# Optimization experiments

Hardware: AMD Instinct MI355X
Metric: run time of the kernel (lower is better)

Reference implementation:

```python
import jax, jax.numpy as jnp
import numpy as np

POOLED_SIZES = [11, 8, 6, 4]
Q_POOLED = 2
NUM_HEADS = 2
EPS_ROUND = 1e-3  # module's self.eps used only in aspect-ratio rounding
LN_EPS = 1e-5     # torch nn.LayerNorm default


def _pool_mat(in_size, out_size):
    # PyTorch adaptive_avg_pool1d windows: start=floor(i*in/out), end=ceil((i+1)*in/out)
    M = np.zeros((out_size, in_size), np.float32)
    for i in range(out_size):
        s = (i * in_size) // out_size
        e = -(((-(i + 1)) * in_size) // out_size)
        M[i, s:e] = 1.0 / (e - s)
    return jnp.asarray(M)


def _bilinear_mat(in_size, out_size):
    # PyTorch F.interpolate bilinear, align_corners=False (half-pixel centers, clamped)
    scale = in_size / out_size
    M = np.zeros((out_size, in_size), np.float32)
    for i in range(out_size):
        src = (i + 0.5) * scale - 0.5
        src = min(max(src, 0.0), in_size - 1)
        i0 = int(np.floor(src))
        i1 = min(i0 + 1, in_size - 1)
        w = src - i0
        M[i, i0] += 1.0 - w
        M[i, i1] += w
    return jnp.asarray(M)


def _ln(x, g, b):
    m = jnp.mean(x, axis=-1, keepdims=True)
    v = jnp.mean((x - m) ** 2, axis=-1, keepdims=True)
    return (x - m) * jax.lax.rsqrt(v + LN_EPS) * g + b


def _out_size(p, H, W):
    if W >= H:
        return (p, round(W * p / H + EPS_ROUND))
    return (round(H * p / W + EPS_ROUND), p)


def setup_inputs() -> dict:
    key = jax.random.key(0)
    ks = jax.random.split(key, 12)
    B, C, H, W = 8, 32, 512, 512
    L = len(POOLED_SIZES)
    return {
        "x": jax.random.normal(ks[0], (B, C, H, W), jnp.float32),
        "q_w": jax.random.normal(ks[1], (C, C), jnp.float32) * 0.05,
        "q_b": jax.random.normal(ks[2], (C,), jnp.float32) * 0.01,
        "kv_w": jax.random.normal(ks[3], (C, 2 * C), jnp.float32) * 0.05,
        "kv_b": jax.random.normal(ks[4], (2 * C,), jnp.float32) * 0.01,
        "proj_w": jax.random.normal(ks[5], (C, C), jnp.float32) * 0.05,
        "proj_b": jax.random.normal(ks[6], (C,), jnp.float32) * 0.01,
        "norm_g": jnp.ones((C,), jnp.float32),
        "norm_b": jnp.zeros((C,), jnp.float32),
        "dconv_w": jax.random.normal(ks[7], (L, C, 1, 3, 3), jnp.float32) * 0.05,  # OIHW depthwise, stacked per level
        "dconv_b": jax.random.normal(ks[8], (L, C), jnp.float32) * 0.01,
        "H": 512,
        "W": 512,
    }


def reference(x, q_w, q_b, kv_w, kv_b, proj_w, proj_b, norm_g, norm_b, dconv_w, dconv_b, H, W):
    B, C = x.shape[0], x.shape[1]
    nh = NUM_HEADS
    hd = C // nh
    scale = hd ** (-0.5)

    # ---- query branch: adaptive pool to ~2x2, then linear ----
    qh, qw = _out_size(Q_POOLED, H, W)
    qp = jnp.einsum('ph,bchw,qw->bcpq', _pool_mat(H, qh), x, _pool_mat(W, qw))  # (B,C,qh,qw)
    qt = qp.reshape(B, C, -1).transpose(0, 2, 1)                               # (B,Nq,C)
    q = (qt @ q_w + q_b).reshape(B, -1, nh, hd).transpose(0, 2, 1, 3)          # (B,nh,Nq,hd)

    # ---- KV pyramid: adaptive pool + depthwise conv residual per level ----
    toks = []
    for i, p in enumerate(POOLED_SIZES):
        ph, pw = _out_size(p, H, W)
        pooled = jnp.einsum('ph,bchw,qw->bcpq', _pool_mat(H, ph), x, _pool_mat(W, pw))
        conv = jax.lax.conv_general_dilated(
            pooled, dconv_w[i], window_strides=(1, 1), padding='SAME',
            feature_group_count=C, dimension_numbers=('NCHW', 'OIHW', 'NCHW'))
        conv = conv + dconv_b[i][None, :, None, None]
        toks.append((pooled + conv).reshape(B, C, -1))
    toks = jnp.concatenate(toks, axis=2).transpose(0, 2, 1)  # (B,Nk,C), Nk=237
    toks = _ln(toks, norm_g, norm_b)

    kv = (toks @ kv_w + kv_b).reshape(B, -1, 2, nh, hd).transpose(2, 0, 3, 1, 4)
    k, v = kv[0], kv[1]                                       # (B,nh,Nk,hd)

    # ---- small-scale attention ----
    attn = jax.nn.softmax(jnp.einsum('bhqd,bhkd->bhqk', q, k) * scale, axis=-1)
    o = jnp.einsum('bhqk,bhkd->bhqd', attn, v).transpose(0, 2, 1, 3).reshape(B, -1, C)
    o = o @ proj_w + proj_b                                    # (B,Nq,C)

    # ---- bilinear upsample back to (H,W) ----
    o = o.transpose(0, 2, 1).reshape(B, C, qh, qw)
    out = jnp.einsum('hp,bcpq,wq->bchw', _bilinear_mat(qh, H), o, _bilinear_mat(qw, W))
    return out  # (B,C,H,W), same as module's to_4d output
```

## Files before the change

kernel.cpp:

```cpp
#include <hip/hip_runtime.h>
#include <math.h>

#define BB 8
#define CC 32
#define NTOK 241
#define NKV 237
#define YW 516
#define NSLOT 16

struct WS { int idx, s, e, left, slot; float ax, ay, az, aw; };

template <int P>
__device__ __forceinline__ void ws_init(WS& w, int i0, int n, int sb) {
  w.idx = i0;
  w.s = (i0 * 512) / P;
  w.e = ((i0 + 1) * 512 + P - 1) / P;
  w.left = n;
  w.slot = sb;
  w.ax = w.ay = w.az = w.aw = 0.f;
}

template <int P>
__device__ __forceinline__ void ws_step(WS& w, float4 v, int r,
                                        float* __restrict__ Y, int c4) {
  if (w.left > 0) {
    if (r >= w.s && r < w.e) {
      w.ax += v.x; w.ay += v.y; w.az += v.z; w.aw += v.w;
    }
    if (r < w.e && r + 4 >= w.e) {
      float* dst = Y + w.slot * YW + c4;
      atomicAdd(dst + 0, w.ax);
      atomicAdd(dst + 1, w.ay);
      atomicAdd(dst + 2, w.az);
      atomicAdd(dst + 3, w.aw);
      w.slot++; w.left--; w.idx++;
      int sn = (w.idx * 512) / P;
      w.e = ((w.idx + 1) * 512 + P - 1) / P;
      bool ov = (sn <= r);
      w.ax = ov ? v.x : 0.f; w.ay = ov ? v.y : 0.f;
      w.az = ov ? v.z : 0.f; w.aw = ov ? v.w : 0.f;
      w.s = sn;
    }
  }
}

__global__ __launch_bounds__(512) void pool_kernel(const float* __restrict__ x,
                                                   float* __restrict__ pooled) {
  __shared__ float Ybuf[NSLOT * YW];

  const int plane = blockIdx.x >> 1;
  const int q = blockIdx.x & 1;
  const int tid = threadIdx.x;

  for (int i = tid; i < NSLOT * YW; i += 512) Ybuf[i] = 0.f;

  const int lo = q ? 256 : 0;
  const int NIT = q ? 64 : 72;
  int i0_2, n_2, i0_11, n_11, i0_8, n_8, i0_6, n_6, i0_4, n_4;
  if (q == 0) {
    i0_2 = 0; n_2 = 1; i0_11 = 0; n_11 = 6; i0_8 = 0; n_8 = 4;
    i0_6 = 0; n_6 = 3; i0_4 = 0; n_4 = 2;
  } else {
    i0_2 = 1; n_2 = 1; i0_11 = 6; n_11 = 5; i0_8 = 4; n_8 = 4;
    i0_6 = 3; n_6 = 3; i0_4 = 2; n_4 = 2;
  }

  WS W2, W11, W8, W6, W4;
  ws_init<2>(W2, i0_2, n_2, 0);
  ws_init<11>(W11, i0_11, n_11, 1);
  ws_init<8>(W8, i0_8, n_8, 7);
  ws_init<6>(W6, i0_6, n_6, 11);
  ws_init<4>(W4, i0_4, n_4, 14);

  const int r0 = tid >> 7;
  const int c4 = (tid & 127) * 4;
  const float* xp = x + (size_t)plane * (512 * 512);

  __syncthreads();

#define LOADIT(IT) \
  (*(const float4*)(xp + (size_t)min(lo + r0 + 4 * (IT), 511) * 512 + c4))
#define PROCIT(V, IT)                                                          \
  {                                                                            \
    int r = lo + r0 + 4 * (IT);                                                \
    ws_step<2>(W2, V, r, Ybuf, c4);                                            \
    ws_step<11>(W11, V, r, Ybuf, c4);                                          \
    ws_step<8>(W8, V, r, Ybuf, c4);                                            \
    ws_step<6>(W6, V, r, Ybuf, c4);                                            \
    ws_step<4>(W4, V, r, Ybuf, c4);                                            \
  }

  float4 Av = LOADIT(0), Bv = LOADIT(1), Cv = LOADIT(2), Dv = LOADIT(3);
  for (int it = 0; it < NIT; it += 4) {
    PROCIT(Av, it);     Av = LOADIT(it + 4);
    PROCIT(Bv, it + 1); Bv = LOADIT(it + 5);
    PROCIT(Cv, it + 2); Cv = LOADIT(it + 6);
    PROCIT(Dv, it + 3); Dv = LOADIT(it + 7);
  }
#undef LOADIT
#undef PROCIT
  __syncthreads();

  const int Ps[5]  = {2, 11, 8, 6, 4};
  const int KBs[5] = {0, 4, 125, 189, 225};
  const int SBs[5] = {0, 1, 7, 11, 14};
  const int i0s[5] = {i0_2, i0_11, i0_8, i0_6, i0_4};
  const int ns[5]  = {n_2, n_11, n_8, n_6, n_4};
  int cum[6]; cum[0] = 0;
#pragma unroll
  for (int l = 0; l < 5; ++l) cum[l + 1] = cum[l] + ns[l] * Ps[l];

  if (tid < cum[5]) {
    int l = 0;
    while (tid >= cum[l + 1]) ++l;
    int P = Ps[l];
    int rel = tid - cum[l];
    int li = rel / P, j = rel - li * P;
    int i = i0s[l] + li;
    int s = (i * 512) / P, e = ((i + 1) * 512 + P - 1) / P;
    int sw = (j * 512) / P, ew = ((j + 1) * 512 + P - 1) / P;
    const float* row = &Ybuf[(SBs[l] + li) * YW];
    float t0 = 0.f, t1 = 0.f, t2 = 0.f, t3 = 0.f;
    int cc = sw;
    for (; cc + 4 <= ew; cc += 4) {
      t0 += row[cc]; t1 += row[cc + 1]; t2 += row[cc + 2]; t3 += row[cc + 3];
    }
    for (; cc < ew; ++cc) t0 += row[cc];
    float val = ((t0 + t1) + (t2 + t3)) / (float)((e - s) * (ew - sw));
    pooled[(size_t)plane * NTOK + KBs[l] + i * P + j] = val;
  }
}

__global__ __launch_bounds__(512) void attn_kernel(
    const float* __restrict__ pooled,
    const float* __restrict__ q_w, const float* __restrict__ q_b,
    const float* __restrict__ kv_w, const float* __restrict__ kv_b,
    const float* __restrict__ proj_w, const float* __restrict__ proj_b,
    const float* __restrict__ norm_g, const float* __restrict__ norm_b,
    const float* __restrict__ dconv_w, const float* __restrict__ dconv_b,
    float* __restrict__ o_out) {
  __shared__ float pl[CC * NTOK];
  __shared__ float toks[NKV][33];
  __shared__ float kvls[NKV][65];
  __shared__ float kvw[CC * 64];
  __shared__ float dw[4 * CC * 9];
  __shared__ float dbias[4 * CC];
  __shared__ float qbias[CC], kvb[64], gln[CC], bln[CC];
  __shared__ float qtok[4][CC];
  __shared__ float attno[4][33];

  const int b = blockIdx.x, tid = threadIdx.x;
  const float* plg = pooled + (size_t)b * CC * NTOK;
  for (int i = tid; i < CC * NTOK; i += 512) pl[i] = plg[i];
  for (int i = tid; i < CC * 64; i += 512) kvw[i] = kv_w[i];
  for (int i = tid; i < 4 * CC * 9; i += 512) dw[i] = dconv_w[i];
  if (tid < 4 * CC) dbias[tid] = dconv_b[tid];
  if (tid < CC) { qbias[tid] = q_b[tid]; gln[tid] = norm_g[tid]; bln[tid] = norm_b[tid]; }
  if (tid >= 64 && tid < 128) kvb[tid - 64] = kv_b[tid - 64];
  __syncthreads();

  for (int item = tid; item < NKV * CC; item += 512) {
    int t = item >> 5, c = item & 31;
    int l, p, kb_, tb;
    if (t < 121)      { l = 0; p = 11; kb_ = 4;   tb = 0; }
    else if (t < 185) { l = 1; p = 8;  kb_ = 125; tb = 121; }
    else if (t < 221) { l = 2; p = 6;  kb_ = 189; tb = 185; }
    else              { l = 3; p = 4;  kb_ = 225; tb = 221; }
    int ti = t - tb;
    int i = ti / p, j = ti - i * p;
    const float* plc = pl + c * NTOK + kb_;
    const float* w9 = dw + (l * CC + c) * 9;
    float acc = dbias[l * CC + c];
#pragma unroll
    for (int dy = -1; dy <= 1; ++dy)
#pragma unroll
      for (int dx = -1; dx <= 1; ++dx) {
        int ii = i + dy, jj = j + dx;
        if (ii >= 0 && ii < p && jj >= 0 && jj < p)
          acc += w9[(dy + 1) * 3 + (dx + 1)] * plc[ii * p + jj];
      }
    toks[t][c] = plc[i * p + j] + acc;
  }
  __syncthreads();

  if (tid < NKV) {
    float xv[32]; float m = 0.f;
#pragma unroll
    for (int c = 0; c < 32; ++c) { xv[c] = toks[tid][c]; m += xv[c]; }
    m *= (1.0f / 32.0f);
    float v = 0.f;
#pragma unroll
    for (int c = 0; c < 32; ++c) { float d = xv[c] - m; v += d * d; }
    v *= (1.0f / 32.0f);
    float rs = rsqrtf(v + 1e-5f);
#pragma unroll
    for (int c = 0; c < 32; ++c) toks[tid][c] = (xv[c] - m) * rs * gln[c] + bln[c];
  } else if (tid >= 384) {
    int it = tid - 384;
    int n = it >> 5, u = it & 31;
    float acc = qbias[u];
#pragma unroll
    for (int c = 0; c < 32; ++c) acc += pl[c * NTOK + n] * q_w[c * 32 + u];
    qtok[n][u] = acc * 0.25f;
  }
  __syncthreads();

  for (int item = tid; item < NKV * 64; item += 512) {
    int t = item >> 6, u = item & 63;
    float acc = kvb[u];
#pragma unroll
    for (int c = 0; c < 32; ++c) acc += toks[t][c] * kvw[c * 64 + u];
    kvls[t][u] = acc;
  }
  __syncthreads();

  {
    int wave = tid >> 6, lane = tid & 63;
    int h = wave >> 2, qi = wave & 3;
    float qv[16];
#pragma unroll
    for (int d = 0; d < 16; ++d) qv[d] = qtok[qi][h * 16 + d];
    float sc[4];
#pragma unroll
    for (int m = 0; m < 4; ++m) {
      int t = lane + m * 64;
      float s = -1e30f;
      if (t < NKV) {
        s = 0.f;
#pragma unroll
        for (int d = 0; d < 16; ++d) s += qv[d] * kvls[t][h * 16 + d];
      }
      sc[m] = s;
    }
    float mx = fmaxf(fmaxf(sc[0], sc[1]), fmaxf(sc[2], sc[3]));
#pragma unroll
    for (int d = 1; d < 64; d <<= 1) mx = fmaxf(mx, __shfl_xor(mx, d));
    float pr[4]; float ssum = 0.f;
#pragma unroll
    for (int m = 0; m < 4; ++m) {
      int t = lane + m * 64;
      pr[m] = (t < NKV) ? expf(sc[m] - mx) : 0.0f;
      ssum += pr[m];
    }
#pragma unroll
    for (int d = 1; d < 64; d <<= 1) ssum += __shfl_xor(ssum, d);
    float acc[16];
#pragma unroll
    for (int d = 0; d < 16; ++d) acc[d] = 0.f;
#pragma unroll
    for (int m = 0; m < 4; ++m) {
      int t = lane + m * 64;
      if (t < NKV) {
        float p = pr[m];
#pragma unroll
        for (int d = 0; d < 16; ++d) acc[d] += p * kvls[t][32 + h * 16 + d];
      }
    }
#pragma unroll
    for (int d = 0; d < 16; ++d) {
#pragma unroll
      for (int s = 1; s < 64; s <<= 1) acc[d] += __shfl_xor(acc[d], s);
    }
    if (lane == 0) {
      float inv = 1.0f / ssum;
#pragma unroll
      for (int d = 0; d < 16; ++d) attno[qi][h * 16 + d] = acc[d] * inv;
    }
  }
  __syncthreads();

  if (tid < 128) {
    int n = tid >> 5, u = tid & 31;
    float acc = proj_b[u];
#pragma unroll
    for (int c = 0; c < 32; ++c) acc += attno[n][c] * proj_w[c * 32 + u];
    o_out[((size_t)b * 32 + u) * 4 + n] = acc;
  }
}

__global__ __launch_bounds__(256) void upsample_kernel(const float* __restrict__ o_in,
                                                       float* __restrict__ out) {
  const int plane = blockIdx.x >> 3;
  const int chunk = blockIdx.x & 7;
  const int tid = threadIdx.x;
  const int sub = tid >> 7, col4 = tid & 127;

  const float o00 = o_in[plane * 4 + 0];
  const float o01 = o_in[plane * 4 + 1];
  const float o10 = o_in[plane * 4 + 2];
  const float o11 = o_in[plane * 4 + 3];

  float top[4], bot[4];
#pragma unroll
  for (int k = 0; k < 4; ++k) {
    float c = (float)(4 * col4 + k) + 0.5f;
    float ww = c * (1.0f / 256.0f) - 0.5f;
    ww = fminf(fmaxf(ww, 0.0f), 1.0f);
    top[k] = o00 + ww * (o01 - o00);
    bot[k] = o10 + ww * (o11 - o10);
  }
  float* outp = out + (size_t)plane * (512 * 512);
  const int r0 = chunk * 64;
  for (int i = 0; i < 32; ++i) {
    int r = r0 + 2 * i + sub;
    float wh = ((float)r + 0.5f) * (1.0f / 256.0f) - 0.5f;
    wh = fminf(fmaxf(wh, 0.0f), 1.0f);
    float4 v;
    v.x = top[0] + wh * (bot[0] - top[0]);
    v.y = top[1] + wh * (bot[1] - top[1]);
    v.z = top[2] + wh * (bot[2] - top[2]);
    v.w = top[3] + wh * (bot[3] - top[3]);
    *(float4*)(outp + r * 512 + 4 * col4) = v;
  }
}

extern "C" void kernel_launch(void* const* d_in, const int* in_sizes, int n_in,
                              void* d_out, int out_size, void* d_ws, size_t ws_size,
                              hipStream_t stream) {
  const float* x       = (const float*)d_in[0];
  const float* q_w     = (const float*)d_in[1];
  const float* q_b     = (const float*)d_in[2];
  const float* kv_w    = (const float*)d_in[3];
  const float* kv_b    = (const float*)d_in[4];
  const float* proj_w  = (const float*)d_in[5];
  const float* proj_b  = (const float*)d_in[6];
  const float* norm_g  = (const float*)d_in[7];
  const float* norm_b  = (const float*)d_in[8];
  const float* dconv_w = (const float*)d_in[9];
  const float* dconv_b = (const float*)d_in[10];
  float* out = (float*)d_out;

  float* pooled = (float*)d_ws;
  float* o_ws   = pooled + (size_t)BB * CC * NTOK;

  pool_kernel<<<BB * CC * 2, 512, 0, stream>>>(x, pooled);
  attn_kernel<<<BB, 512, 0, stream>>>(pooled, q_w, q_b, kv_w, kv_b, proj_w,
                                      proj_b, norm_g, norm_b, dconv_w, dconv_b,
                                      o_ws);
  upsample_kernel<<<BB * CC * 8, 256, 0, stream>>>(o_ws, out);
}
```

Baseline: 222.4 us.

## Pool whole plane per block with staggered start rows; grid-stride upsample

```diff
diff --git a/kernel.cpp b/kernel.cpp
--- a/kernel.cpp
+++ b/kernel.cpp
@@ -6,128 +6,119 @@
 #define NTOK 241
 #define NKV 237
 #define YW 516
-#define NSLOT 16
-
-struct WS { int idx, s, e, left, slot; float ax, ay, az, aw; };
-
-template <int P>
-__device__ __forceinline__ void ws_init(WS& w, int i0, int n, int sb) {
-  w.idx = i0;
-  w.s = (i0 * 512) / P;
-  w.e = ((i0 + 1) * 512 + P - 1) / P;
-  w.left = n;
-  w.slot = sb;
-  w.ax = w.ay = w.az = w.aw = 0.f;
-}
-
-template <int P>
-__device__ __forceinline__ void ws_step(WS& w, float4 v, int r,
-                                        float* __restrict__ Y, int c4) {
-  if (w.left > 0) {
-    if (r >= w.s && r < w.e) {
-      w.ax += v.x; w.ay += v.y; w.az += v.z; w.aw += v.w;
-    }
-    if (r < w.e && r + 4 >= w.e) {
-      float* dst = Y + w.slot * YW + c4;
-      atomicAdd(dst + 0, w.ax);
-      atomicAdd(dst + 1, w.ay);
-      atomicAdd(dst + 2, w.az);
-      atomicAdd(dst + 3, w.aw);
-      w.slot++; w.left--; w.idx++;
-      int sn = (w.idx * 512) / P;
-      w.e = ((w.idx + 1) * 512 + P - 1) / P;
-      bool ov = (sn <= r);
-      w.ax = ov ? v.x : 0.f; w.ay = ov ? v.y : 0.f;
-      w.az = ov ? v.z : 0.f; w.aw = ov ? v.w : 0.f;
-      w.s = sn;
-    }
-  }
-}
+
+template <int P, int NW, int SB>
+struct WM {
+  int idx, s, e;
+  float ax, ay, az, aw;
+  __device__ __forceinline__ void init(int row) {
+    idx = (row * P) >> 9;
+    s = (idx * 512) / P;
+    e = ((idx + 1) * 512 + P - 1) / P;
+    ax = ay = az = aw = 0.f;
+  }
+  __device__ __forceinline__ void flush(float* __restrict__ Y, int c4) {
+    if (idx < NW) {
+      float* dst = Y + (SB + idx) * YW + c4;
+      atomicAdd(dst + 0, ax);
+      atomicAdd(dst + 1, ay);
+      atomicAdd(dst + 2, az);
+      atomicAdd(dst + 3, aw);
+    }
+  }
+  __device__ __forceinline__ void step(float4 v, int r, float* __restrict__ Y,
+                                       int c4) {
+    if (r >= s && r < e) { ax += v.x; ay += v.y; az += v.z; aw += v.w; }
+    if (r < e && r + 4 >= e) {
+      flush(Y, c4);
+      idx++;
+      int sn = (idx * 512) / P;
+      e = ((idx + 1) * 512 + P - 1) / P;
+      bool ov = (sn <= r) && (idx < NW);
+      ax = ov ? v.x : 0.f; ay = ov ? v.y : 0.f;
+      az = ov ? v.z : 0.f; aw = ov ? v.w : 0.f;
+      s = sn;
+    }
+  }
+};
 
 __global__ __launch_bounds__(512) void pool_kernel(const float* __restrict__ x,
                                                    float* __restrict__ pooled) {
-  __shared__ float Ybuf[NSLOT * YW];
-
-  const int plane = blockIdx.x >> 1;
-  const int q = blockIdx.x & 1;
+  __shared__ float Ybuf[31 * YW];
+
+  const int plane = blockIdx.x;
   const int tid = threadIdx.x;
-
-  for (int i = tid; i < NSLOT * YW; i += 512) Ybuf[i] = 0.f;
-
-  const int lo = q ? 256 : 0;
-  const int NIT = q ? 64 : 72;
-  int i0_2, n_2, i0_11, n_11, i0_8, n_8, i0_6, n_6, i0_4, n_4;
-  if (q == 0) {
-    i0_2 = 0; n_2 = 1; i0_11 = 0; n_11 = 6; i0_8 = 0; n_8 = 4;
-    i0_6 = 0; n_6 = 3; i0_4 = 0; n_4 = 2;
-  } else {
-    i0_2 = 1; n_2 = 1; i0_11 = 6; n_11 = 5; i0_8 = 4; n_8 = 4;
-    i0_6 = 3; n_6 = 3; i0_4 = 2; n_4 = 2;
-  }
-
-  WS W2, W11, W8, W6, W4;
-  ws_init<2>(W2, i0_2, n_2, 0);
-  ws_init<11>(W11, i0_11, n_11, 1);
-  ws_init<8>(W8, i0_8, n_8, 7);
-  ws_init<6>(W6, i0_6, n_6, 11);
-  ws_init<4>(W4, i0_4, n_4, 14);
-
   const int r0 = tid >> 7;
   const int c4 = (tid & 127) * 4;
   const float* xp = x + (size_t)plane * (512 * 512);
 
-  __syncthreads();
-
-#define LOADIT(IT) \
-  (*(const float4*)(xp + (size_t)min(lo + r0 + 4 * (IT), 511) * 512 + c4))
+  for (int i = tid; i < 31 * YW; i += 512) Ybuf[i] = 0.f;
+
+  const int off = (plane * 73) & 511;
+  int i_w = (512 - off - r0 + 3) >> 2;
+  if (i_w > 128) i_w = 128;
+  const int row0 = (off + r0) & 511;
+
+  WM<2, 2, 0> M2;    M2.init(row0);
+  WM<11, 11, 2> M11; M11.init(row0);
+  WM<8, 8, 13> M8;   M8.init(row0);
+  WM<6, 6, 21> M6;   M6.init(row0);
+  WM<4, 4, 27> M4;   M4.init(row0);
+
+  __syncthreads();
+
+#define ROWOF(IT) ((off + r0 + 4 * (IT)) & 511)
+#define LOADIT(IT) (*(const float4*)(xp + (size_t)ROWOF(IT) * 512 + c4))
+#define FLUSHALL                                                               \
+  { M2.flush(Ybuf, c4); M11.flush(Ybuf, c4); M8.flush(Ybuf, c4);               \
+    M6.flush(Ybuf, c4); M4.flush(Ybuf, c4); }
+#define REINIT(ROW)                                                            \
+  { M2.init(ROW); M11.init(ROW); M8.init(ROW); M6.init(ROW); M4.init(ROW); }
 #define PROCIT(V, IT)                                                          \
   {                                                                            \
-    int r = lo + r0 + 4 * (IT);                                                \
-    ws_step<2>(W2, V, r, Ybuf, c4);                                            \
-    ws_step<11>(W11, V, r, Ybuf, c4);                                          \
-    ws_step<8>(W8, V, r, Ybuf, c4);                                            \
-    ws_step<6>(W6, V, r, Ybuf, c4);                                            \
-    ws_step<4>(W4, V, r, Ybuf, c4);                                            \
+    if ((IT) == i_w) { FLUSHALL; REINIT(ROWOF(IT)); }                          \
+    int r = ROWOF(IT);                                                         \
+    M2.step(V, r, Ybuf, c4);                                                   \
+    M11.step(V, r, Ybuf, c4);                                                  \
+    M8.step(V, r, Ybuf, c4);                                                   \
+    M6.step(V, r, Ybuf, c4);                                                   \
+    M4.step(V, r, Ybuf, c4);                                                   \
   }
 
   float4 Av = LOADIT(0), Bv = LOADIT(1), Cv = LOADIT(2), Dv = LOADIT(3);
-  for (int it = 0; it < NIT; it += 4) {
+  for (int it = 0; it < 128; it += 4) {
     PROCIT(Av, it);     Av = LOADIT(it + 4);
     PROCIT(Bv, it + 1); Bv = LOADIT(it + 5);
     PROCIT(Cv, it + 2); Cv = LOADIT(it + 6);
     PROCIT(Dv, it + 3); Dv = LOADIT(it + 7);
   }
+  FLUSHALL;
+#undef ROWOF
 #undef LOADIT
+#undef FLUSHALL
+#undef REINIT
 #undef PROCIT
   __syncthreads();
 
-  const int Ps[5]  = {2, 11, 8, 6, 4};
-  const int KBs[5] = {0, 4, 125, 189, 225};
-  const int SBs[5] = {0, 1, 7, 11, 14};
-  const int i0s[5] = {i0_2, i0_11, i0_8, i0_6, i0_4};
-  const int ns[5]  = {n_2, n_11, n_8, n_6, n_4};
-  int cum[6]; cum[0] = 0;
-#pragma unroll
-  for (int l = 0; l < 5; ++l) cum[l + 1] = cum[l] + ns[l] * Ps[l];
-
-  if (tid < cum[5]) {
-    int l = 0;
-    while (tid >= cum[l + 1]) ++l;
-    int P = Ps[l];
-    int rel = tid - cum[l];
-    int li = rel / P, j = rel - li * P;
-    int i = i0s[l] + li;
-    int s = (i * 512) / P, e = ((i + 1) * 512 + P - 1) / P;
-    int sw = (j * 512) / P, ew = ((j + 1) * 512 + P - 1) / P;
-    const float* row = &Ybuf[(SBs[l] + li) * YW];
+  if (tid < NTOK) {
+    int k = tid, p, sbase, kb;
+    if (k < 4)        { p = 2;  sbase = 0;  kb = 0; }
+    else if (k < 125) { p = 11; sbase = 2;  kb = 4; }
+    else if (k < 189) { p = 8;  sbase = 13; kb = 125; }
+    else if (k < 225) { p = 6;  sbase = 21; kb = 189; }
+    else              { p = 4;  sbase = 27; kb = 225; }
+    int idx = k - kb, i = idx / p, j = idx - i * p;
+    int si = (i * 512) / p, ei = ((i + 1) * 512 + p - 1) / p;
+    int sw = (j * 512) / p, ew = ((j + 1) * 512 + p - 1) / p;
+    const float* row = &Ybuf[(sbase + i) * YW];
     float t0 = 0.f, t1 = 0.f, t2 = 0.f, t3 = 0.f;
     int cc = sw;
     for (; cc + 4 <= ew; cc += 4) {
       t0 += row[cc]; t1 += row[cc + 1]; t2 += row[cc + 2]; t3 += row[cc + 3];
     }
     for (; cc < ew; ++cc) t0 += row[cc];
-    float val = ((t0 + t1) + (t2 + t3)) / (float)((e - s) * (ew - sw));
-    pooled[(size_t)plane * NTOK + KBs[l] + i * P + j] = val;
+    float val = ((t0 + t1) + (t2 + t3)) / (float)((ei - si) * (ew - sw));
+    pooled[(size_t)plane * NTOK + k] = val;
   }
 }
 
@@ -280,37 +271,36 @@
 
 __global__ __launch_bounds__(256) void upsample_kernel(const float* __restrict__ o_in,
                                                        float* __restrict__ out) {
-  const int plane = blockIdx.x >> 3;
-  const int chunk = blockIdx.x & 7;
   const int tid = threadIdx.x;
-  const int sub = tid >> 7, col4 = tid & 127;
-
-  const float o00 = o_in[plane * 4 + 0];
-  const float o01 = o_in[plane * 4 + 1];
-  const float o10 = o_in[plane * 4 + 2];
-  const float o11 = o_in[plane * 4 + 3];
-
-  float top[4], bot[4];
-#pragma unroll
-  for (int k = 0; k < 4; ++k) {
-    float c = (float)(4 * col4 + k) + 0.5f;
-    float ww = c * (1.0f / 256.0f) - 0.5f;
-    ww = fminf(fmaxf(ww, 0.0f), 1.0f);
-    top[k] = o00 + ww * (o01 - o00);
-    bot[k] = o10 + ww * (o11 - o10);
-  }
-  float* outp = out + (size_t)plane * (512 * 512);
-  const int r0 = chunk * 64;
-  for (int i = 0; i < 32; ++i) {
-    int r = r0 + 2 * i + sub;
+  const int wv = tid >> 6, lane = tid & 63;
+  const int gw0 = blockIdx.x * 4 + wv;
+
+  float ww[8];
+#pragma unroll
+  for (int k = 0; k < 8; ++k) {
+    float cx = (float)(lane * 8 + k) + 0.5f;
+    float w = cx * (1.0f / 256.0f) - 0.5f;
+    ww[k] = fminf(fmaxf(w, 0.0f), 1.0f);
+  }
+
+  for (int g = gw0; g < 256 * 512; g += 4096) {
+    int plane = g >> 9, r = g & 511;
+    float o00 = o_in[plane * 4 + 0];
+    float o01 = o_in[plane * 4 + 1];
+    float o10 = o_in[plane * 4 + 2];
+    float o11 = o_in[plane * 4 + 3];
     float wh = ((float)r + 0.5f) * (1.0f / 256.0f) - 0.5f;
     wh = fminf(fmaxf(wh, 0.0f), 1.0f);
-    float4 v;
-    v.x = top[0] + wh * (bot[0] - top[0]);
-    v.y = top[1] + wh * (bot[1] - top[1]);
-    v.z = top[2] + wh * (bot[2] - top[2]);
-    v.w = top[3] + wh * (bot[3] - top[3]);
-    *(float4*)(outp + r * 512 + 4 * col4) = v;
+    float v[8];
+#pragma unroll
+    for (int k = 0; k < 8; ++k) {
+      float t = o00 + ww[k] * (o01 - o00);
+      float bb = o10 + ww[k] * (o11 - o10);
+      v[k] = t + wh * (bb - t);
+    }
+    float* op = out + (size_t)g * 512 + lane * 8;
+    *(float4*)op = make_float4(v[0], v[1], v[2], v[3]);
+    *(float4*)(op + 4) = make_float4(v[4], v[5], v[6], v[7]);
   }
 }
 
@@ -333,9 +323,9 @@
   float* pooled = (float*)d_ws;
   float* o_ws   = pooled + (size_t)BB * CC * NTOK;
 
-  pool_kernel<<<BB * CC * 2, 512, 0, stream>>>(x, pooled);
+  pool_kernel<<<BB * CC, 512, 0, stream>>>(x, pooled);
   attn_kernel<<<BB, 512, 0, stream>>>(pooled, q_w, q_b, kv_w, kv_b, proj_w,
                                       proj_b, norm_g, norm_b, dconv_w, dconv_b,
                                       o_ws);
-  upsample_kernel<<<BB * CC * 8, 256, 0, stream>>>(o_ws, out);
+  upsample_kernel<<<1024, 256, 0, stream>>>(o_ws, out);
 }
```

Result: slower. 301.9 us (+35.8%).
